# Kernel optimization log

Measured on AMD Instinct MI355X. Metric: run time of the kernel, lower is better.

## Reference

```python
import jax, jax.numpy as jnp
import numpy as np

IN_DIM = 256
OUT_DIM = 256
EMBED_DIM = 256
GROUPS = 8
BN_EPS = 1e-5


def conv2d(x, w, b, pad, groups=1):
    # x: NCHW, w: OIHW (I = in_ch / groups)
    out = jax.lax.conv_general_dilated(
        x, w, window_strides=(1, 1), padding=[(pad, pad), (pad, pad)],
        dimension_numbers=('NCHW', 'OIHW', 'NCHW'), feature_group_count=groups)
    return out + b[None, :, None, None]


def setup_inputs() -> dict:
    key = jax.random.key(0)
    ks = jax.random.split(key, 8)
    s = 0.05
    d = {}
    d['x'] = jax.random.normal(ks[0], (2, IN_DIM, 16, 16), jnp.float32)
    d['y'] = jax.random.normal(ks[1], (2, OUT_DIM, 128, 128), jnp.float32)
    # channle_reduce: Conv2d(256, 64, k=3, groups=64) -> weight (64, 4, 3, 3)
    d['w_cr'] = jax.random.normal(ks[2], (IN_DIM // 4, 4, 3, 3), jnp.float32) * s
    d['b_cr'] = jnp.zeros((IN_DIM // 4,), jnp.float32)
    # depthwise convs on 64 channels
    d['w_dw3'] = jax.random.normal(ks[3], (IN_DIM // 4, 1, 3, 3), jnp.float32) * s
    d['b_dw3'] = jnp.zeros((IN_DIM // 4,), jnp.float32)
    d['w_dw7'] = jax.random.normal(ks[4], (IN_DIM // 4, 1, 5, 5), jnp.float32) * s
    d['b_dw7'] = jnp.zeros((IN_DIM // 4,), jnp.float32)
    # gate: Conv2d(256, 128, 1) + BN + StarReLU
    d['w_gate'] = jax.random.normal(ks[5], (IN_DIM // 2, IN_DIM, 1, 1), jnp.float32) * s
    d['b_gate'] = jnp.zeros((IN_DIM // 2,), jnp.float32)
    d['bn_gamma'] = jnp.ones((IN_DIM // 2,), jnp.float32)
    d['bn_beta'] = jnp.zeros((IN_DIM // 2,), jnp.float32)
    d['bn_mean'] = jnp.zeros((IN_DIM // 2,), jnp.float32)
    d['bn_var'] = jnp.ones((IN_DIM // 2,), jnp.float32)
    d['sr_scale'] = jnp.ones((1,), jnp.float32)
    d['sr_bias'] = jnp.zeros((1,), jnp.float32)
    # linear1: Linear(16, 8192) -> torch weight shape (8192, 16)
    d['w_lin'] = jax.random.normal(ks[6], (OUT_DIM * EMBED_DIM // GROUPS, IN_DIM // (2 * GROUPS)), jnp.float32) * s
    d['b_lin'] = jnp.zeros((OUT_DIM * EMBED_DIM // GROUPS,), jnp.float32)
    return d


def reference(x, y, w_cr, b_cr, w_dw3, b_dw3, w_dw7, b_dw7, w_gate, b_gate,
              bn_gamma, bn_beta, bn_mean, bn_var, sr_scale, sr_bias, w_lin, b_lin):
    B, C, H, Wd = x.shape
    # gate branch: 1x1 conv -> BN (inference stats) -> StarReLU
    g = conv2d(x, w_gate, b_gate, 0)
    inv = (bn_gamma / jnp.sqrt(bn_var + BN_EPS))[None, :, None, None]
    g = (g - bn_mean[None, :, None, None]) * inv + bn_beta[None, :, None, None]
    g = sr_scale * jnp.square(jnp.maximum(g, 0.0)) + sr_bias
    # feature branch
    xr = conv2d(x, w_cr, b_cr, 1, groups=IN_DIM // 4)        # (B, 64, H, W)
    x3 = conv2d(xr, w_dw3, b_dw3, 1, groups=IN_DIM // 4)
    x7 = conv2d(xr, w_dw7, b_dw7, 2, groups=IN_DIM // 4)
    xc = jnp.concatenate([x3, x7], axis=1) * g               # (B, 128, H, W)
    # per-pixel weight generation: (B,H,W,G,16) @ (16,8192)
    xc = xc.reshape(B, GROUPS, -1, H, Wd).transpose(0, 3, 4, 1, 2)
    wdec = jnp.einsum('bhwgi,oi->bhwgo', xc, w_lin) + b_lin  # (B,H,W,8,8192)
    # flatten (G, out*embed/G) -> (embed, out); matches torch reshape order
    wdec = wdec.reshape(B, H, Wd, EMBED_DIM, OUT_DIM)
    # patch-wise dynamic 1x1 conv == per-patch batched matmul
    b, c, h, w = y.shape
    fh, fw = H, Wd
    ph, pw = h // fh, w // fw
    yp = y.reshape(b, c, fh, ph, fw, pw)
    # out[b,e,f,p,g,q] = sum_c wdec[b,f,g,e,c] * y[b,c,f,p,g,q]
    out = jnp.einsum('bfgec,bcfpgq->befpgq', wdec, yp)
    return out.reshape(b, EMBED_DIM, h, w)
```

## Files before the change

kernel.cpp:

```cpp
#include <hip/hip_runtime.h>
#include <stdint.h>


typedef __attribute__((ext_vector_type(8))) short short8;
typedef __attribute__((ext_vector_type(4))) float f32x4;

#define BN_EPS 1e-5f

__device__ __forceinline__ unsigned short f2bf(float f) {
  unsigned u = __float_as_uint(f);
  return (unsigned short)((u + 0x8000u) >> 16);
}
__device__ __forceinline__ unsigned pk2bf(float a, float b) {
  unsigned ua = __float_as_uint(a), ub = __float_as_uint(b);
  return ((ua + 0x8000u) >> 16) | ((ub + 0x8000u) & 0xFFFF0000u);
}

__global__ __launch_bounds__(256) void k1a_groupconv(
    const float* __restrict__ x, const float* __restrict__ w_cr,
    const float* __restrict__ b_cr, float* __restrict__ xr)
{
  __shared__ float xs[4][256];
  int b = blockIdx.x >> 6, cr = blockIdx.x & 63;
  int t = threadIdx.x;
  {
    int ch = t >> 6, off = (t & 63) * 4;
    float4 v = *(const float4*)(x + b * 65536 + (cr * 4 + ch) * 256 + off);
    *(float4*)&xs[ch][off] = v;
  }
  __syncthreads();
  int h = t >> 4, w = t & 15;
  float a = b_cr[cr];
  #pragma unroll
  for (int ii = 0; ii < 4; ++ii) {
    const float* wp = w_cr + (cr * 4 + ii) * 9;
    #pragma unroll
    for (int ky = 0; ky < 3; ++ky) {
      int gy = h + ky - 1;
      #pragma unroll
      for (int kx = 0; kx < 3; ++kx) {
        int gx = w + kx - 1;
        float v = (gy >= 0 && gy < 16 && gx >= 0 && gx < 16) ? xs[ii][gy * 16 + gx] : 0.f;
        a += wp[ky * 3 + kx] * v;
      }
    }
  }
  xr[(b * 64 + cr) * 256 + t] = a;
}

__global__ __launch_bounds__(256) void k1b_gate_dw(
    const float* __restrict__ x, const float* __restrict__ xr,
    const float* __restrict__ w_dw3, const float* __restrict__ b_dw3,
    const float* __restrict__ w_dw7, const float* __restrict__ b_dw7,
    const float* __restrict__ w_gate, const float* __restrict__ b_gate,
    const float* __restrict__ bn_gamma, const float* __restrict__ bn_beta,
    const float* __restrict__ bn_mean, const float* __restrict__ bn_var,
    const float* __restrict__ sr_scale, const float* __restrict__ sr_bias,
    const float* __restrict__ w_lin, short* __restrict__ wlin_bf, short* __restrict__ xc_bf)
{
  __shared__ float xcen[256];
  __shared__ float gs[128];
  int blk = blockIdx.x;
  int b = blk >> 8, h = (blk >> 4) & 15, w = blk & 15;
  int t = threadIdx.x;

  { int idx = blk * 256 + t; wlin_bf[idx] = (short)f2bf(w_lin[idx]); }

  xcen[t] = x[b * 65536 + t * 256 + h * 16 + w];
  __syncthreads();

  int o = t >> 1, half = t & 1;
  {
    const float* wrow = w_gate + o * 256 + half * 128;
    const float* xcn  = xcen + half * 128;
    float ga = 0.f;
    #pragma unroll 8
    for (int ci = 0; ci < 128; ci += 4) {
      float4 wv = *(const float4*)(wrow + ci);
      float4 xv = *(const float4*)(xcn + ci);
      ga += wv.x * xv.x + wv.y * xv.y + wv.z * xv.z + wv.w * xv.w;
    }
    ga += __shfl_xor(ga, 1);
    float inv = bn_gamma[o] * rsqrtf(bn_var[o] + BN_EPS);
    float gg = (ga + b_gate[o] - bn_mean[o]) * inv + bn_beta[o];
    gg = fmaxf(gg, 0.f);
    gg = sr_scale[0] * gg * gg + sr_bias[0];
    if (half == 0) gs[o] = gg;
  }
  __syncthreads();

  if (t < 128) {
    int oc = t;
    float f0;
    if (oc < 64) {
      f0 = b_dw3[oc];
      const float* wp = w_dw3 + oc * 9;
      const float* xp = xr + (b * 64 + oc) * 256;
      #pragma unroll
      for (int ky = 0; ky < 3; ++ky) {
        int gy = h + ky - 1;
        #pragma unroll
        for (int kx = 0; kx < 3; ++kx) {
          int gx = w + kx - 1;
          float v = (gy >= 0 && gy < 16 && gx >= 0 && gx < 16) ? xp[gy * 16 + gx] : 0.f;
          f0 += wp[ky * 3 + kx] * v;
        }
      }
    } else {
      int c5 = oc - 64;
      f0 = b_dw7[c5];
      const float* wp = w_dw7 + c5 * 25;
      const float* xp = xr + (b * 64 + c5) * 256;
      #pragma unroll
      for (int ky = 0; ky < 5; ++ky) {
        int gy = h + ky - 2;
        #pragma unroll
        for (int kx = 0; kx < 5; ++kx) {
          int gx = w + kx - 2;
          float v = (gy >= 0 && gy < 16 && gx >= 0 && gx < 16) ? xp[gy * 5 * 0 + gy * 16 + gx] : 0.f;
          f0 += wp[ky * 5 + kx] * v;
        }
      }
    }
    int pix = (b * 16 + h) * 16 + w;
    xc_bf[pix * 128 + oc] = (short)f2bf(f0 * gs[oc]);
  }
}

__global__ __launch_bounds__(256) void k2a_wgen(
    const short* __restrict__ wlin_bf, const short* __restrict__ xc_bf,
    const float* __restrict__ b_lin, short* __restrict__ wd)
{
  int blk = blockIdx.x;
  int n0 = (blk >> 2) * 16;
  int tid = threadIdx.x;
  int wave = tid >> 6, lane = tid & 63;
  int quad = lane >> 4, l16 = lane & 15;
  int obase = (blk & 3) * 2048 + wave * 512;

  short8 af = {0, 0, 0, 0, 0, 0, 0, 0};
  if (quad < 2) af = *(const short8*)(xc_bf + (n0 + l16) * 16 + quad * 8);

  f32x4 zero4 = {0.f, 0.f, 0.f, 0.f};
  #pragma unroll 8
  for (int i = 0; i < 32; ++i) {
    int o0 = obase + i * 16;
    short8 bf = {0, 0, 0, 0, 0, 0, 0, 0};
    if (quad < 2) bf = *(const short8*)(wlin_bf + (o0 + l16) * 16 + quad * 8);
    f32x4 d = __builtin_amdgcn_mfma_f32_16x16x32_bf16(af, bf, zero4, 0, 0, 0);
    float bl = b_lin[o0 + l16];
    short* wp = wd + (size_t)(n0 + quad * 4) * 8192 + o0 + l16;
    #pragma unroll
    for (int r = 0; r < 4; ++r)
      wp[(size_t)r * 8192] = (short)f2bf(d[r] + bl);
  }
}

__global__ __launch_bounds__(512, 4) void k2b_dynconv(
    const float* __restrict__ y, const short* __restrict__ wd,
    float* __restrict__ out)
{
  __shared__ __align__(16) short Ylds[16384];
  __shared__ __align__(16) float scratch[8192];

  int phys = blockIdx.x;
  int blk = (phys & 7) * 64 + (phys >> 3);
  int b = blk >> 8, f = (blk >> 4) & 15, g = blk & 15;
  int tid = threadIdx.x;
  int wave = tid >> 6, lane = tid & 63;
  int quad = lane >> 4, l16 = lane & 15;

  const float* yb = y + b * 4194304 + (f * 8) * 128 + g * 8;
  const short* wdp = wd + (size_t)(((b * 16 + f) * 16 + g)) * 65536;

  int c32 = tid >> 4, pf = tid & 15;
  for (int sch = 0; sch < 2; ++sch) {
    float4 v[4];
    #pragma unroll
    for (int it = 0; it < 4; ++it)
      v[it] = *(const float4*)(yb + (sch * 128 + it * 32 + c32) * 16384 + (pf >> 1) * 128 + (pf & 1) * 4);
    #pragma unroll
    for (int it = 0; it < 4; ++it)
      *(float4*)&scratch[(it * 32 + c32) * 64 + pf * 4] = v[it];
    __syncthreads();
    #pragma unroll
    for (int tt = 0; tt < 2; ++tt) {
      int task = tt * 512 + tid;
      int pix = task & 63, cg = task >> 6;
      float s0 = scratch[(cg * 8 + 0) * 64 + pix];
      float s1 = scratch[(cg * 8 + 1) * 64 + pix];
      float s2 = scratch[(cg * 8 + 2) * 64 + pix];
      float s3 = scratch[(cg * 8 + 3) * 64 + pix];
      float s4 = scratch[(cg * 8 + 4) * 64 + pix];
      float s5 = scratch[(cg * 8 + 5) * 64 + pix];
      float s6 = scratch[(cg * 8 + 6) * 64 + pix];
      float s7 = scratch[(cg * 8 + 7) * 64 + pix];
      uint4 pk;
      pk.x = pk2bf(s0, s1); pk.y = pk2bf(s2, s3);
      pk.z = pk2bf(s4, s5); pk.w = pk2bf(s6, s7);
      int chunk = sch * 16 + cg;
      int physc = chunk ^ (pix & 7);
      *(uint4*)&Ylds[pix * 256 + physc * 8] = pk;
    }
    __syncthreads();
  }

  f32x4 acc[2][4];
  f32x4 zero4 = {0.f, 0.f, 0.f, 0.f};
  #pragma unroll
  for (int et = 0; et < 2; ++et)
    #pragma unroll
    for (int nt = 0; nt < 4; ++nt)
      acc[et][nt] = zero4;

  #pragma unroll 2
  for (int cc = 0; cc < 8; ++cc) {
    short8 A[2], Bf[4];
    #pragma unroll
    for (int et = 0; et < 2; ++et) {
      int e = wave * 32 + et * 16 + l16;
      A[et] = *(const short8*)(wdp + e * 256 + cc * 32 + quad * 8);
    }
    int chunk = cc * 4 + quad;
    #pragma unroll
    for (int nt = 0; nt < 4; ++nt) {
      int nn = nt * 16 + l16;
      int physc = chunk ^ (nn & 7);
      Bf[nt] = *(const short8*)&Ylds[nn * 256 + physc * 8];
    }
    #pragma unroll
    for (int et = 0; et < 2; ++et)
      #pragma unroll
      for (int nt = 0; nt < 4; ++nt)
        acc[et][nt] = __builtin_amdgcn_mfma_f32_16x16x32_bf16(A[et], Bf[nt], acc[et][nt], 0, 0, 0);
  }

  float* ob = out + b * 4194304 + (f * 8) * 128 + g * 8;
  #pragma unroll
  for (int et = 0; et < 2; ++et) {
    int e0 = wave * 32 + et * 16 + quad * 4;
    #pragma unroll
    for (int nt = 0; nt < 4; ++nt) {
      int pix = nt * 16 + l16;
      float* oa = ob + (pix >> 3) * 128 + (pix & 7);
      #pragma unroll
      for (int r = 0; r < 4; ++r)
        oa[(e0 + r) * 16384] = acc[et][nt][r];
    }
  }
}

extern "C" void kernel_launch(void* const* d_in, const int* in_sizes, int n_in,
                              void* d_out, int out_size, void* d_ws, size_t ws_size,
                              hipStream_t stream) {
  const float* x        = (const float*)d_in[0];
  const float* y        = (const float*)d_in[1];
  const float* w_cr     = (const float*)d_in[2];
  const float* b_cr     = (const float*)d_in[3];
  const float* w_dw3    = (const float*)d_in[4];
  const float* b_dw3    = (const float*)d_in[5];
  const float* w_dw7    = (const float*)d_in[6];
  const float* b_dw7    = (const float*)d_in[7];
  const float* w_gate   = (const float*)d_in[8];
  const float* b_gate   = (const float*)d_in[9];
  const float* bn_gamma = (const float*)d_in[10];
  const float* bn_beta  = (const float*)d_in[11];
  const float* bn_mean  = (const float*)d_in[12];
  const float* bn_var   = (const float*)d_in[13];
  const float* sr_scale = (const float*)d_in[14];
  const float* sr_bias  = (const float*)d_in[15];
  const float* w_lin    = (const float*)d_in[16];
  const float* b_lin    = (const float*)d_in[17];
  float* out = (float*)d_out;

  short* xc_bf   = (short*)d_ws;
  short* wlin_bf = (short*)((char*)d_ws + 131072);
  float* xr      = (float*)((char*)d_ws + 131072 + 262144);
  short* wd      = (short*)((char*)d_ws + 131072 + 262144 + 131072);

  hipLaunchKernelGGL(k1a_groupconv, dim3(128), dim3(256), 0, stream, x, w_cr, b_cr, xr);
  hipLaunchKernelGGL(k1b_gate_dw, dim3(512), dim3(256), 0, stream,
                     x, xr, w_dw3, b_dw3, w_dw7, b_dw7, w_gate, b_gate,
                     bn_gamma, bn_beta, bn_mean, bn_var, sr_scale, sr_bias,
                     w_lin, wlin_bf, xc_bf);
  hipLaunchKernelGGL(k2a_wgen, dim3(1024), dim3(256), 0, stream,
                     wlin_bf, xc_bf, b_lin, wd);
  hipLaunchKernelGGL(k2b_dynconv, dim3(512), dim3(512), 0, stream, y, wd, out);
}
```

Baseline: 164.4 us.

## Fuse per-pixel weight generation into dynamic conv kernel via double-buffered LDS

The separate weight-generation kernel that wrote a 64 MB bf16 per-pixel weight tensor to global memory is removed. The dynamic-conv kernel now computes each 32-channel chunk of the per-patch 256x256 weight matrix on the fly with MFMA, writes it into a swizzled, double-buffered LDS region reused from the scratch buffer, and consumes it in the next step. This removes a large global write and re-read. In exchange it adds redundant wlin loads, extra MFMAs per block and a barrier per chunk iteration.

Result: slower. 168.4 us (+2.4%).

```diff
diff --git a/kernel.cpp b/kernel.cpp
--- a/kernel.cpp
+++ b/kernel.cpp
@@ -117,7 +117,7 @@
         #pragma unroll
         for (int kx = 0; kx < 5; ++kx) {
           int gx = w + kx - 2;
-          float v = (gy >= 0 && gy < 16 && gx >= 0 && gx < 16) ? xp[gy * 5 * 0 + gy * 16 + gx] : 0.f;
+          float v = (gy >= 0 && gy < 16 && gx >= 0 && gx < 16) ? xp[gy * 16 + gx] : 0.f;
           f0 += wp[ky * 5 + kx] * v;
         }
       }
@@ -127,41 +127,14 @@
   }
 }
 
-__global__ __launch_bounds__(256) void k2a_wgen(
-    const short* __restrict__ wlin_bf, const short* __restrict__ xc_bf,
-    const float* __restrict__ b_lin, short* __restrict__ wd)
-{
-  int blk = blockIdx.x;
-  int n0 = (blk >> 2) * 16;
-  int tid = threadIdx.x;
-  int wave = tid >> 6, lane = tid & 63;
-  int quad = lane >> 4, l16 = lane & 15;
-  int obase = (blk & 3) * 2048 + wave * 512;
-
-  short8 af = {0, 0, 0, 0, 0, 0, 0, 0};
-  if (quad < 2) af = *(const short8*)(xc_bf + (n0 + l16) * 16 + quad * 8);
-
-  f32x4 zero4 = {0.f, 0.f, 0.f, 0.f};
-  #pragma unroll 8
-  for (int i = 0; i < 32; ++i) {
-    int o0 = obase + i * 16;
-    short8 bf = {0, 0, 0, 0, 0, 0, 0, 0};
-    if (quad < 2) bf = *(const short8*)(wlin_bf + (o0 + l16) * 16 + quad * 8);
-    f32x4 d = __builtin_amdgcn_mfma_f32_16x16x32_bf16(af, bf, zero4, 0, 0, 0);
-    float bl = b_lin[o0 + l16];
-    short* wp = wd + (size_t)(n0 + quad * 4) * 8192 + o0 + l16;
-    #pragma unroll
-    for (int r = 0; r < 4; ++r)
-      wp[(size_t)r * 8192] = (short)f2bf(d[r] + bl);
-  }
-}
-
-__global__ __launch_bounds__(512, 4) void k2b_dynconv(
-    const float* __restrict__ y, const short* __restrict__ wd,
+__global__ __launch_bounds__(512, 4) void k2_fused(
+    const float* __restrict__ y, const short* __restrict__ wlin_bf,
+    const short* __restrict__ xc_bf, const float* __restrict__ b_lin,
     float* __restrict__ out)
 {
   __shared__ __align__(16) short Ylds[16384];
   __shared__ __align__(16) float scratch[8192];
+  short* wdlds = (short*)scratch;
 
   int phys = blockIdx.x;
   int blk = (phys & 7) * 64 + (phys >> 3);
@@ -171,7 +144,6 @@
   int quad = lane >> 4, l16 = lane & 15;
 
   const float* yb = y + b * 4194304 + (f * 8) * 128 + g * 8;
-  const short* wdp = wd + (size_t)(((b * 16 + f) * 16 + g)) * 65536;
 
   int c32 = tid >> 4, pf = tid & 15;
   for (int sch = 0; sch < 2; ++sch) {
@@ -205,34 +177,71 @@
     __syncthreads();
   }
 
+  short8 bx = {0, 0, 0, 0, 0, 0, 0, 0};
+  if (quad < 2 && l16 < 8)
+    bx = *(const short8*)(xc_bf + blk * 128 + l16 * 16 + quad * 8);
+
+  f32x4 zero4 = {0.f, 0.f, 0.f, 0.f};
   f32x4 acc[2][4];
-  f32x4 zero4 = {0.f, 0.f, 0.f, 0.f};
   #pragma unroll
   for (int et = 0; et < 2; ++et)
     #pragma unroll
     for (int nt = 0; nt < 4; ++nt)
       acc[et][nt] = zero4;
 
-  #pragma unroll 2
+  auto gen_chunk = [&](int cc, int buf) {
+    short* dst = wdlds + buf * 8192;
+    #pragma unroll
+    for (int jj = 0; jj < 4; ++jj) {
+      int j = wave * 4 + jj;
+      #pragma unroll
+      for (int hh = 0; hh < 2; ++hh) {
+        int c0 = cc * 32 + hh * 16;
+        short8 aw = {0, 0, 0, 0, 0, 0, 0, 0};
+        if (quad < 2)
+          aw = *(const short8*)(wlin_bf + (j * 256 + c0 + l16) * 16 + quad * 8);
+        f32x4 d = __builtin_amdgcn_mfma_f32_16x16x32_bf16(aw, bx, zero4, 0, 0, 0);
+        if (l16 < 8) {
+          int e = l16 * 32 + j;
+          float4 bl = *(const float4*)(b_lin + j * 256 + c0 + quad * 4);
+          uint2 pk;
+          pk.x = pk2bf(d[0] + bl.x, d[1] + bl.y);
+          pk.y = pk2bf(d[2] + bl.z, d[3] + bl.w);
+          int q16 = hh * 2 + (quad >> 1);
+          int sw = q16 ^ ((e >> 1) & 3) ^ ((e >> 5) & 3);
+          *(uint2*)&dst[e * 32 + sw * 8 + (quad & 1) * 4] = pk;
+        }
+      }
+    }
+  };
+
+  gen_chunk(0, 0);
+  __syncthreads();
+
   for (int cc = 0; cc < 8; ++cc) {
-    short8 A[2], Bf[4];
+    if (cc < 7) gen_chunk(cc + 1, (cc + 1) & 1);
+
+    const short* src = wdlds + (cc & 1) * 8192;
+    short8 A2[2], Bf[4];
     #pragma unroll
     for (int et = 0; et < 2; ++et) {
       int e = wave * 32 + et * 16 + l16;
-      A[et] = *(const short8*)(wdp + e * 256 + cc * 32 + quad * 8);
-    }
-    int chunk = cc * 4 + quad;
+      int sw = quad ^ ((e >> 1) & 3) ^ ((e >> 5) & 3);
+      A2[et] = *(const short8*)&src[e * 32 + sw * 8];
+    }
+    int chunkY = cc * 4 + quad;
     #pragma unroll
     for (int nt = 0; nt < 4; ++nt) {
       int nn = nt * 16 + l16;
-      int physc = chunk ^ (nn & 7);
+      int physc = chunkY ^ (nn & 7);
       Bf[nt] = *(const short8*)&Ylds[nn * 256 + physc * 8];
     }
     #pragma unroll
     for (int et = 0; et < 2; ++et)
       #pragma unroll
       for (int nt = 0; nt < 4; ++nt)
-        acc[et][nt] = __builtin_amdgcn_mfma_f32_16x16x32_bf16(A[et], Bf[nt], acc[et][nt], 0, 0, 0);
+        acc[et][nt] = __builtin_amdgcn_mfma_f32_16x16x32_bf16(A2[et], Bf[nt], acc[et][nt], 0, 0, 0);
+    __syncthreads();
   }
 
   float* ob = out + b * 4194304 + (f * 8) * 128 + g * 8;
@@ -276,14 +285,12 @@
   short* xc_bf   = (short*)d_ws;
   short* wlin_bf = (short*)((char*)d_ws + 131072);
   float* xr      = (float*)((char*)d_ws + 131072 + 262144);
-  short* wd      = (short*)((char*)d_ws + 131072 + 262144 + 131072);
 
   hipLaunchKernelGGL(k1a_groupconv, dim3(128), dim3(256), 0, stream, x, w_cr, b_cr, xr);
   hipLaunchKernelGGL(k1b_gate_dw, dim3(512), dim3(256), 0, stream,
                      x, xr, w_dw3, b_dw3, w_dw7, b_dw7, w_gate, b_gate,
                      bn_gamma, bn_beta, bn_mean, bn_var, sr_scale, sr_bias,
                      w_lin, wlin_bf, xc_bf);
-  hipLaunchKernelGGL(k2a_wgen, dim3(1024), dim3(256), 0, stream,
-                     wlin_bf, xc_bf, b_lin, wd);
-  hipLaunchKernelGGL(k2b_dynconv, dim3(512), dim3(512), 0, stream, y, wd, out);
-}
+  hipLaunchKernelGGL(k2_fused, dim3(512), dim3(512), 0, stream,
+                     y, wlin_bf, xc_bf, b_lin, out);
+}
```
